# Optimization experiments

Measured on AMD Instinct MI355X. Metric: run time of the kernel, lower is better.

The kernel has to match this reference:

```python
import jax, jax.numpy as jnp
import numpy as np

L = 16          # num_slices
RMIN, RMAX = 0.4, 0.9
B_, C_, H_, W_, N_ = 2, 4, 64, 64, 64   # n = 64 scan steps, last dim of x = N_*L


def setup_inputs() -> dict:
    key = jax.random.key(0)
    k = jax.random.split(key, 8)
    u1 = jax.random.uniform(k[0], (L,), dtype=jnp.float32)
    u2 = jax.random.uniform(k[1], (L,), dtype=jnp.float32)
    theta = 2.0 * np.pi * u2
    nu_log = jnp.log(-0.5 * jnp.log(u1 * (RMAX ** 2 - RMIN ** 2) + RMIN ** 2))
    # torch.complex(exp(-exp(nu_log)), theta): real part = modulus-like term, imag = theta
    Lambda_re = jnp.exp(-jnp.exp(nu_log))
    Lambda_im = theta
    B_re = jax.random.normal(k[2], (L, L), dtype=jnp.float32)
    B_im = jax.random.normal(k[3], (L, L), dtype=jnp.float32)
    C_re = jax.random.normal(k[4], (L, L), dtype=jnp.float32)
    C_im = jax.random.normal(k[5], (L, L), dtype=jnp.float32)
    D = jax.random.normal(k[6], (L, L), dtype=jnp.float32)
    x = jax.random.normal(k[7], (B_, C_, H_, W_, N_ * L), dtype=jnp.float32)
    return {"x": x, "Lambda_re": Lambda_re, "Lambda_im": Lambda_im,
            "B_re": B_re, "B_im": B_im, "C_re": C_re, "C_im": C_im, "D": D}


def reference(x, Lambda_re, Lambda_im, B_re, B_im, C_re, C_im, D):
    l = Lambda_re.shape[0]
    b, c, h, w, nl = x.shape
    n = nl // l
    img = x.reshape(b, c, h, w, n, l)                       # 'b c h w (n l) -> b c h w n l'
    Lam = jax.lax.complex(Lambda_re, Lambda_im)             # (l,) complex64
    Bc = jax.lax.complex(B_re, B_im)                        # (l,l) complex64
    Cc = jax.lax.complex(C_re, C_im)
    out = img.astype(jnp.complex64)
    # Faithful Hillis-Steele loop with op(x, y) = Lambda*x + B @ y
    for d in range(1, int(np.log2(n)) + 1):
        step = 2 ** (d - 1)
        left = out[..., : n - step, :]
        right = out[..., step:, :]
        new = left * Lam + jnp.einsum('kl,bchwnl->bchwnk', Bc, right)
        out = jnp.concatenate([out[..., :step, :], new], axis=-2)
    y = jnp.real(jnp.einsum('kl,bchwnl->bchwnk', Cc, out)) \
        + jnp.einsum('kl,bchwnl->bchwnk', D, img)
    return y
```

## Files before the change

### kernel.cpp

```cpp
#include <hip/hip_runtime.h>


namespace {

typedef __attribute__((ext_vector_type(8))) short short8v;
typedef __attribute__((ext_vector_type(4))) float f32x4;

__device__ inline unsigned short f2bf_rne(float f) {
    unsigned u = __builtin_bit_cast(unsigned, f);
    u += 0x7fffu + ((u >> 16) & 1u);
    return (unsigned short)(u >> 16);
}

__device__ inline void gld_lds16(const unsigned short* g, unsigned short* l) {
    __builtin_amdgcn_global_load_lds(
        (const __attribute__((address_space(1))) unsigned int*)g,
        (__attribute__((address_space(3))) unsigned int*)l, 16, 0, 0);
}


__global__ __launch_bounds__(256) void build_w_kernel(
    const float* __restrict__ Lre, const float* __restrict__ Lim,
    const float* __restrict__ Bre, const float* __restrict__ Bim,
    const float* __restrict__ Cre, const float* __restrict__ Cim,
    const float* __restrict__ Dm,
    unsigned short* __restrict__ Wh)
{
    const int i = blockIdx.x >> 6, j = blockIdx.x & 63;
    const int t = threadIdx.x, k = t >> 4, l = t & 15;

    const int n_g = i * 16 + k;
    const int k_g = j * 16 + l;
    const size_t widx = (((size_t)((n_g >> 8) * 32 + (k_g >> 5))) << 13)
                      + (((k_g >> 3) & 3) << 11) + ((n_g & 255) << 3) + (k_g & 7);

    if (j > i) { Wh[widx] = 0; return; }

    __shared__ float2 Bs[16][16];
    __shared__ float2 M[16][16];
    Bs[k][l] = make_float2(Bre[t], Bim[t]);
    M[k][l]  = make_float2(k == l ? 1.f : 0.f, 0.f);
    const int delta = i - j;
    __syncthreads();

    #pragma unroll
    for (int d = 0; d < 6; ++d) {
        const int s = 1 << d;
        if (delta & s) {
            const float lr = Lre[k], li = Lim[k];
            const float2 m0 = M[k][l];
            M[k][l] = make_float2(lr * m0.x - li * m0.y, lr * m0.y + li * m0.x);
            __syncthreads();
        } else if (j + (delta & (s - 1)) >= s) {
            float2 acc = make_float2(0.f, 0.f);
            #pragma unroll
            for (int m = 0; m < 16; ++m) {
                const float2 b = Bs[k][m], v = M[m][l];
                acc.x += b.x * v.x - b.y * v.y;
                acc.y += b.x * v.y + b.y * v.x;
            }
            __syncthreads();
            M[k][l] = acc;
            __syncthreads();
        }
    }

    float w = 0.f;
    #pragma unroll
    for (int m = 0; m < 16; ++m) {
        const float2 v = M[m][l];
        w += Cre[k * 16 + m] * v.x - Cim[k * 16 + m] * v.y;
    }
    if (i == j) w += Dm[t];
    Wh[widx] = f2bf_rne(w);
}

__global__ __launch_bounds__(256) void gemm_fused_kernel(
    const float* __restrict__ X,
    const unsigned short* __restrict__ Wh,
    float* __restrict__ Y, int mtiles)
{
    __shared__ alignas(16) float sA[2][4096];
    __shared__ alignas(16) unsigned short sB[2][8192];

    const int bid = blockIdx.x;
    const int sb = 3 - bid / mtiles;
    const int mt = bid % mtiles;
    const int t = threadIdx.x;
    const int wid = t >> 6, lane = t & 63;
    const int wr = wid >> 1, wc = wid & 1;
    const int l15 = lane & 15, lg = lane >> 4;
    const int nt = (sb + 1) * 8;

    f32x4 acc[4][8] = {};

    int arow[4], as0[4], as1[4];
    #pragma unroll
    for (int mm = 0; mm < 4; ++mm) {
        const int row = wr * 64 + mm * 16 + l15;
        arow[mm] = row << 5;
        as0[mm] = (((2 * lg)     ^ (row & 7)) << 2);
        as1[mm] = (((2 * lg + 1) ^ (row & 7)) << 2);
    }
    int bfo[8];
    #pragma unroll
    for (int nn = 0; nn < 8; ++nn)
        bfo[nn] = (lg << 11) + ((wc * 128 + nn * 16 + l15) << 3);

    auto stageT = [&](int b, int tk) {
        float* bA = sA[b];
        unsigned short* bB = sB[b];
        const float* xbase = X + (size_t)mt * 131072 + tk * 32;
        #pragma unroll
        for (int p = 0; p < 4; ++p) {
            const int s = p * 256 + t;
            const int row = s >> 3, kq = s & 7;
            const float* src = xbase + (size_t)row * 1024 + ((kq ^ (row & 7)) << 2);
            gld_lds16((const unsigned short*)src, (unsigned short*)(bA + s * 4));
        }
        const unsigned short* wb = Wh + (((size_t)(sb * 32 + tk)) << 13);
        #pragma unroll
        for (int p = 0; p < 4; ++p) {
            const int e8 = (p * 256 + t) * 8;
            gld_lds16(wb + e8, bB + e8);
        }
    };

    stageT(0, 0);
    __syncthreads();

    for (int tk = 0; tk < nt; ++tk) {
        const int c = tk & 1;
        if (tk + 1 < nt) stageT(c ^ 1, tk + 1);

        short8v ah[4];
        #pragma unroll
        for (int mm = 0; mm < 4; ++mm) {
            const f32x4 q0 = *reinterpret_cast<const f32x4*>(sA[c] + arow[mm] + as0[mm]);
            const f32x4 q1 = *reinterpret_cast<const f32x4*>(sA[c] + arow[mm] + as1[mm]);
            short8v r;
            r[0] = (short)f2bf_rne(q0[0]); r[1] = (short)f2bf_rne(q0[1]);
            r[2] = (short)f2bf_rne(q0[2]); r[3] = (short)f2bf_rne(q0[3]);
            r[4] = (short)f2bf_rne(q1[0]); r[5] = (short)f2bf_rne(q1[1]);
            r[6] = (short)f2bf_rne(q1[2]); r[7] = (short)f2bf_rne(q1[3]);
            ah[mm] = r;
        }
        short8v bh[8];
        #pragma unroll
        for (int nn = 0; nn < 8; ++nn)
            bh[nn] = *reinterpret_cast<const short8v*>(sB[c] + bfo[nn]);

        __builtin_amdgcn_s_setprio(1);
        #pragma unroll
        for (int mm = 0; mm < 4; ++mm)
            #pragma unroll
            for (int nn = 0; nn < 8; ++nn)
                acc[mm][nn] = __builtin_amdgcn_mfma_f32_16x16x32_bf16(
                    ah[mm], bh[nn], acc[mm][nn], 0, 0, 0);
        __builtin_amdgcn_s_setprio(0);

        __syncthreads();
    }

    #pragma unroll
    for (int mm = 0; mm < 4; ++mm) {
        const int grow = mt * 128 + wr * 64 + mm * 16 + lg * 4;
        #pragma unroll
        for (int nn = 0; nn < 8; ++nn) {
            const int gcol = sb * 256 + wc * 128 + nn * 16 + l15;
            #pragma unroll
            for (int q = 0; q < 4; ++q)
                Y[(size_t)(grow + q) * 1024 + gcol] = acc[mm][nn][q];
        }
    }
}

}

extern "C" void kernel_launch(void* const* d_in, const int* in_sizes, int n_in,
                              void* d_out, int out_size, void* d_ws, size_t ws_size,
                              hipStream_t stream) {
    const float* x   = (const float*)d_in[0];
    const float* Lre = (const float*)d_in[1];
    const float* Lim = (const float*)d_in[2];
    const float* Bre = (const float*)d_in[3];
    const float* Bim = (const float*)d_in[4];
    const float* Cre = (const float*)d_in[5];
    const float* Cim = (const float*)d_in[6];
    const float* Dm  = (const float*)d_in[7];
    float* y = (float*)d_out;

    const int positions = in_sizes[0] / 1024;
    const int mtiles = positions / 128;

    unsigned short* Wh = (unsigned short*)d_ws;

    build_w_kernel<<<4096, 256, 0, stream>>>(Lre, Lim, Bre, Bim, Cre, Cim, Dm, Wh);
    gemm_fused_kernel<<<mtiles * 4, 256, 0, stream>>>(x, Wh, y, mtiles);
}
```

Baseline: 96.26 us.

## Triple-buffer X tiles with fine-grained vmcnt waits and packed bf16 conversion

```diff
diff --git a/kernel.cpp b/kernel.cpp
--- a/kernel.cpp
+++ b/kernel.cpp
@@ -1,10 +1,12 @@
 #include <hip/hip_runtime.h>
+#include <hip/hip_bf16.h>
 
 
 namespace {
 
 typedef __attribute__((ext_vector_type(8))) short short8v;
 typedef __attribute__((ext_vector_type(4))) float f32x4;
+typedef __attribute__((ext_vector_type(4))) unsigned uint4v;
 
 __device__ inline unsigned short f2bf_rne(float f) {
     unsigned u = __builtin_bit_cast(unsigned, f);
@@ -16,6 +18,13 @@
     __builtin_amdgcn_global_load_lds(
         (const __attribute__((address_space(1))) unsigned int*)g,
         (__attribute__((address_space(3))) unsigned int*)l, 16, 0, 0);
+}
+
+__device__ inline unsigned pk2(float a, float b) {
+    __hip_bfloat162 h = __float22bfloat162_rn(make_float2(a, b));
+    unsigned r;
+    __builtin_memcpy(&r, &h, 4);
+    return r;
 }
 
 
@@ -75,12 +84,12 @@
     Wh[widx] = f2bf_rne(w);
 }
 
-__global__ __launch_bounds__(256) void gemm_fused_kernel(
+__global__ __launch_bounds__(256, 2) void gemm_fused_kernel(
     const float* __restrict__ X,
     const unsigned short* __restrict__ Wh,
     float* __restrict__ Y, int mtiles)
 {
-    __shared__ alignas(16) float sA[2][4096];
+    __shared__ alignas(16) float sA[3][4096];
     __shared__ alignas(16) unsigned short sB[2][8192];
 
     const int bid = blockIdx.x;
@@ -107,9 +116,8 @@
     for (int nn = 0; nn < 8; ++nn)
         bfo[nn] = (lg << 11) + ((wc * 128 + nn * 16 + l15) << 3);
 
-    auto stageT = [&](int b, int tk) {
+    auto stageA = [&](int b, int tk) {
         float* bA = sA[b];
-        unsigned short* bB = sB[b];
         const float* xbase = X + (size_t)mt * 131072 + tk * 32;
         #pragma unroll
         for (int p = 0; p < 4; ++p) {
@@ -118,6 +126,9 @@
             const float* src = xbase + (size_t)row * 1024 + ((kq ^ (row & 7)) << 2);
             gld_lds16((const unsigned short*)src, (unsigned short*)(bA + s * 4));
         }
+    };
+    auto stageW = [&](int b, int tk) {
+        unsigned short* bB = sB[b];
         const unsigned short* wb = Wh + (((size_t)(sb * 32 + tk)) << 13);
         #pragma unroll
         for (int p = 0; p < 4; ++p) {
@@ -126,29 +137,42 @@
         }
     };
 
-    stageT(0, 0);
-    __syncthreads();
-
+    stageA(0, 0);
+    stageW(0, 0);
+    stageA(1, 1);
+    asm volatile("s_waitcnt vmcnt(4)" ::: "memory");
+    __builtin_amdgcn_sched_barrier(0);
+    __builtin_amdgcn_s_barrier();
+    __builtin_amdgcn_sched_barrier(0);
+
+    int cA = 0, cA2 = 2;
     for (int tk = 0; tk < nt; ++tk) {
-        const int c = tk & 1;
-        if (tk + 1 < nt) stageT(c ^ 1, tk + 1);
+        const int cW = tk & 1;
+        if (tk + 2 < nt) {
+            stageW(cW ^ 1, tk + 1);
+            stageA(cA2, tk + 2);
+        } else if (tk + 1 < nt) {
+            stageW(cW ^ 1, tk + 1);
+        }
 
         short8v ah[4];
         #pragma unroll
         for (int mm = 0; mm < 4; ++mm) {
-            const f32x4 q0 = *reinterpret_cast<const f32x4*>(sA[c] + arow[mm] + as0[mm]);
-            const f32x4 q1 = *reinterpret_cast<const f32x4*>(sA[c] + arow[mm] + as1[mm]);
+            const f32x4 q0 = *reinterpret_cast<const f32x4*>(sA[cA] + arow[mm] + as0[mm]);
+            const f32x4 q1 = *reinterpret_cast<const f32x4*>(sA[cA] + arow[mm] + as1[mm]);
+            uint4v uv;
+            uv[0] = pk2(q0[0], q0[1]);
+            uv[1] = pk2(q0[2], q0[3]);
+            uv[2] = pk2(q1[0], q1[1]);
+            uv[3] = pk2(q1[2], q1[3]);
             short8v r;
-            r[0] = (short)f2bf_rne(q0[0]); r[1] = (short)f2bf_rne(q0[1]);
-            r[2] = (short)f2bf_rne(q0[2]); r[3] = (short)f2bf_rne(q0[3]);
-            r[4] = (short)f2bf_rne(q1[0]); r[5] = (short)f2bf_rne(q1[1]);
-            r[6] = (short)f2bf_rne(q1[2]); r[7] = (short)f2bf_rne(q1[3]);
+            __builtin_memcpy(&r, &uv, 16);
             ah[mm] = r;
         }
         short8v bh[8];
         #pragma unroll
         for (int nn = 0; nn < 8; ++nn)
-            bh[nn] = *reinterpret_cast<const short8v*>(sB[c] + bfo[nn]);
+            bh[nn] = *reinterpret_cast<const short8v*>(sB[cW] + bfo[nn]);
 
         __builtin_amdgcn_s_setprio(1);
         #pragma unroll
@@ -159,7 +183,18 @@
                     ah[mm], bh[nn], acc[mm][nn], 0, 0, 0);
         __builtin_amdgcn_s_setprio(0);
 
-        __syncthreads();
+        if (tk + 1 < nt) {
+            if (tk + 2 < nt) {
+                asm volatile("s_waitcnt vmcnt(4)" ::: "memory");
+            } else {
+                asm volatile("s_waitcnt vmcnt(0)" ::: "memory");
+            }
+            __builtin_amdgcn_sched_barrier(0);
+            __builtin_amdgcn_s_barrier();
+            __builtin_amdgcn_sched_barrier(0);
+        }
+        cA = (cA == 2) ? 0 : cA + 1;
+        cA2 = (cA2 == 2) ? 0 : cA2 + 1;
     }
 
     #pragma unroll
```

Result: no change. 96.67 us (+0.4%).
